# Optimization experiments

Hardware: AMD Instinct MI355X
Metric: run time of the kernel (lower is better)

## Reference

```python
import jax, jax.numpy as jnp
import numpy as np

DIM = 768
NUM_HEADS = 12
HEAD_DIM = DIM // NUM_HEADS
HW = 32  # input_size = (32, 32)


def setup_inputs() -> dict:
    key = jax.random.key(0)
    ks = jax.random.split(key, 7)
    return {
        "x": jax.random.normal(ks[0], (8, HW, HW, DIM), dtype=jnp.float32),
        "w_qkv": jax.random.normal(ks[1], (DIM, 3 * DIM), dtype=jnp.float32) * 0.02,
        "b_qkv": jnp.zeros((3 * DIM,), dtype=jnp.float32),
        "w_proj": jax.random.normal(ks[2], (DIM, DIM), dtype=jnp.float32) * 0.02,
        "b_proj": jnp.zeros((DIM,), dtype=jnp.float32),
        "rel_pos_h": jax.random.normal(ks[3], (2 * HW - 1, HEAD_DIM), dtype=jnp.float32) * 0.02,
        "rel_pos_w": jax.random.normal(ks[4], (2 * HW - 1, HEAD_DIM), dtype=jnp.float32) * 0.02,
    }


def _gather_rel_pos(size, rel_pos):
    # q_size == k_size == size, so no resize; index = i - j + (size - 1)
    idx = jnp.arange(size)[:, None] - jnp.arange(size)[None, :] + (size - 1)
    return rel_pos[idx]  # [size, size, head_dim]


def reference(x, w_qkv, b_qkv, w_proj, b_proj, rel_pos_h, rel_pos_w):
    B, H, W, C = x.shape
    nH, D = NUM_HEADS, HEAD_DIM
    scale = D ** -0.5
    S = H * W

    qkv = x.reshape(B, S, C) @ w_qkv + b_qkv          # [B,S,3C]
    qkv = qkv.reshape(B, S, 3, nH, D).transpose(2, 0, 3, 1, 4)  # [3,B,nH,S,D]
    q, k, v = qkv[0], qkv[1], qkv[2]

    attn = jnp.einsum('bnsd,bntd->bnst', q * scale, k)  # [B,nH,S,S]

    # decomposed relative positional bias
    Rh = _gather_rel_pos(H, rel_pos_h)                  # [H,H,D]
    Rw = _gather_rel_pos(W, rel_pos_w)                  # [W,W,D]
    r_q = q.reshape(B, nH, H, W, D)
    rel_h = jnp.einsum('bnhwc,hkc->bnhwk', r_q, Rh)     # [B,nH,H,W,H]
    rel_w = jnp.einsum('bnhwc,wkc->bnhwk', r_q, Rw)     # [B,nH,H,W,W]
    attn = (attn.reshape(B, nH, H, W, H, W)
            + rel_h[..., :, None]
            + rel_w[..., None, :]).reshape(B, nH, S, S)

    attn = jax.nn.softmax(attn, axis=-1)
    out = jnp.einsum('bnst,bntd->bnsd', attn, v)        # [B,nH,S,D]
    out = out.transpose(0, 2, 1, 3).reshape(B, H, W, C)
    return out @ w_proj + b_proj
```

## Files before the change

### kernel.cpp

```cpp
#include <hip/hip_runtime.h>
#include <cstdint>
#include <cstddef>

#define NH 12
#define HDIM 64
#define C_ 768
#define C3 2304
#define SEQ 1024
#define LS 72
#define LSV 76
#define SMAX 6.0f
#define LOG2E 1.4426950408889634f

typedef short bf16x8_t __attribute__((ext_vector_type(8)));
typedef float f32x4_t __attribute__((ext_vector_type(4)));
typedef unsigned short u16x4_t __attribute__((ext_vector_type(4)));

__device__ __forceinline__ unsigned short bf16_rne(float x) {
    unsigned int u = __float_as_uint(x);
    u += 0x7FFFu + ((u >> 16) & 1u);
    return (unsigned short)(u >> 16);
}
__device__ __forceinline__ float bf16f(unsigned short h) {
    return __uint_as_float(((unsigned int)h) << 16);
}

__device__ __forceinline__ void load_lds16(const unsigned short* g, unsigned short* l) {
    auto gp = (const __attribute__((address_space(1))) unsigned short*)(uintptr_t)g;
    auto lp = (__attribute__((address_space(3))) unsigned short*)(uint32_t)(uintptr_t)l;
    __builtin_amdgcn_global_load_lds(gp, lp, 16, 0, 0);
}

__device__ __forceinline__ int swz(int row, int g) {
    const int pr = row >> 1;
    const int ch = (((row & 1) << 2) | g) ^ (pr & 7);
    return pr * 64 + ch * 8;
}

__global__ __launch_bounds__(256)
void split_kernel(const float* __restrict__ in, unsigned short* __restrict__ hi)
{
    const int i = blockIdx.x * 256 + threadIdx.x;
    float4 v = ((const float4*)in)[i];
    u16x4_t h;
    h.x = bf16_rne(v.x); h.y = bf16_rne(v.y); h.z = bf16_rne(v.z); h.w = bf16_rne(v.w);
    ((u16x4_t*)hi)[i] = h;
}

__global__ __launch_bounds__(256)
void splitT_kernel(const float* __restrict__ W, unsigned short* __restrict__ Thi,
                   unsigned short* __restrict__ Tlo, int Kdim, int Ndim)
{
    __shared__ float tile[32][33];
    const int t = threadIdx.x;
    const int kb = blockIdx.y * 32, nb = blockIdx.x * 32;
    const int lr = t >> 3, lc = (t & 7) * 4;
    *(float4*)&tile[lr][lc] = *(const float4*)&W[(size_t)(kb + lr) * Ndim + nb + lc];
    __syncthreads();
    const float v0 = tile[lc + 0][lr];
    const float v1 = tile[lc + 1][lr];
    const float v2 = tile[lc + 2][lr];
    const float v3 = tile[lc + 3][lr];
    u16x4_t h, l;
    h.x = bf16_rne(v0); l.x = bf16_rne(v0 - bf16f(h.x));
    h.y = bf16_rne(v1); l.y = bf16_rne(v1 - bf16f(h.y));
    h.z = bf16_rne(v2); l.z = bf16_rne(v2 - bf16f(h.z));
    h.w = bf16_rne(v3); l.w = bf16_rne(v3 - bf16f(h.w));
    *(u16x4_t*)&Thi[(size_t)(nb + lr) * Kdim + kb + lc] = h;
    *(u16x4_t*)&Tlo[(size_t)(nb + lr) * Kdim + kb + lc] = l;
}

__global__ __launch_bounds__(256, 2)
void qkvgemm_kernel(const unsigned short* __restrict__ Ahi, const unsigned short* __restrict__ BThi,
                    const float* __restrict__ bias,
                    unsigned short* __restrict__ q_hi, unsigned short* __restrict__ k_hi,
                    unsigned short* __restrict__ v_hi)
{
    constexpr int K = 768;
    __shared__ unsigned short As[4096];
    __shared__ unsigned short Bs[4096];
    const int tid = threadIdx.x;
    const int w = tid >> 6, lane = tid & 63, g = lane >> 4, r = lane & 15;
    const int wr = (w >> 1) * 64, wc = (w & 1) * 64;

    const int bid  = blockIdx.x;
    const int xcd  = bid & 7;
    const int idx  = bid >> 3;
    const int msub = idx & 7;
    const int ntile = idx >> 3;
    const int m0 = (xcd * 8 + msub) * 128;
    const int n0 = ntile * 128;

    int row_[2], gc_[2];
#pragma unroll
    for (int i = 0; i < 2; ++i) {
        const int s = i * 256 + tid;
        const int pr = s >> 3;
        const int u = (s & 7) ^ (pr & 7);
        row_[i] = pr * 2 + (u >> 2);
        gc_[i]  = u & 3;
    }
    const unsigned short* gA0 = Ahi + (size_t)(m0 + row_[0]) * K + gc_[0] * 8;
    const unsigned short* gA1 = Ahi + (size_t)(m0 + row_[1]) * K + gc_[1] * 8;
    const unsigned short* gB0 = BThi + (size_t)(n0 + row_[0]) * K + gc_[0] * 8;
    const unsigned short* gB1 = BThi + (size_t)(n0 + row_[1]) * K + gc_[1] * 8;
    unsigned short* lA0 = As + w * 512;
    unsigned short* lA1 = As + 2048 + w * 512;
    unsigned short* lB0 = Bs + w * 512;
    unsigned short* lB1 = Bs + 2048 + w * 512;

    f32x4_t acc[4][4];
#pragma unroll
    for (int i = 0; i < 4; ++i)
#pragma unroll
        for (int j = 0; j < 4; ++j)
#pragma unroll
            for (int q = 0; q < 4; ++q) acc[i][j][q] = 0.f;

    for (int k0 = 0; k0 < K; k0 += 32) {
        __syncthreads();
        load_lds16(gA0 + k0, lA0);
        load_lds16(gA1 + k0, lA1);
        load_lds16(gB0 + k0, lB0);
        load_lds16(gB1 + k0, lB1);
        __syncthreads();
        bf16x8_t am[4];
#pragma unroll
        for (int i = 0; i < 4; ++i)
            am[i] = *(const bf16x8_t*)&As[swz(wr + 16 * i + r, g)];
#pragma unroll
        for (int j = 0; j < 4; ++j) {
            const bf16x8_t bn = *(const bf16x8_t*)&Bs[swz(wc + 16 * j + r, g)];
#pragma unroll
            for (int i = 0; i < 4; ++i)
                acc[i][j] = __builtin_amdgcn_mfma_f32_16x16x32_bf16(am[i], bn, acc[i][j], 0, 0, 0);
        }
    }

    const int third = n0 >= 1536 ? 2 : (n0 >= 768 ? 1 : 0);
    unsigned short* outH = third == 2 ? v_hi : third == 1 ? k_hi : q_hi;
#pragma unroll
    for (int j = 0; j < 4; ++j) {
        const int n = n0 + wc + 16 * j + r;
        const float bj = bias[n];
        const int nn = n - third * 768;
        const int h = nn >> 6, d = nn & 63;
#pragma unroll
        for (int i = 0; i < 4; ++i) {
            const int m = m0 + wr + 16 * i + 4 * g;
            const int b = m >> 10, t = m & 1023;
            const size_t hb = ((size_t)(b * NH + h)) << 16;
            unsigned short* dh = outH + hb + (size_t)t * 64 + d;
#pragma unroll
            for (int q = 0; q < 4; ++q)
                dh[(size_t)q * 64] = bf16_rne(acc[i][j][q] + bj);
        }
    }
}

template<int N>
__global__ __launch_bounds__(256, 2)
void gemm_mfma_kernel(const unsigned short* __restrict__ Ahi, const unsigned short* __restrict__ Alo,
                      const unsigned short* __restrict__ BThi, const unsigned short* __restrict__ BTlo,
                      const float* __restrict__ bias, float* __restrict__ C)
{
    constexpr int K = 768;
    __shared__ unsigned short As[128 * LS];
    __shared__ unsigned short Bs[128 * LS];
    const int tid = threadIdx.x;
    const int w = tid >> 6, lane = tid & 63, g = lane >> 4, r = lane & 15;
    const int wr = (w >> 1) * 64, wc = (w & 1) * 64;

    const int bid  = blockIdx.x;
    const int xcd  = bid & 7;
    const int idx  = bid >> 3;
    const int msub = idx & 7;
    const int ntile = idx >> 3;
    const int m0 = (xcd * 8 + msub) * 128;
    const int n0 = ntile * 128;

    const int srow = tid >> 1, sh = (tid & 1) * 16;

    const unsigned short* aH = Ahi + (size_t)(m0 + srow) * K + sh;
    const unsigned short* aL = Alo + (size_t)(m0 + srow) * K + sh;
    const unsigned short* bH = BThi + (size_t)(n0 + srow) * K + sh;
    const unsigned short* bL = BTlo + (size_t)(n0 + srow) * K + sh;

    f32x4_t acc[4][4];
#pragma unroll
    for (int i = 0; i < 4; ++i)
#pragma unroll
        for (int j = 0; j < 4; ++j)
#pragma unroll
            for (int q = 0; q < 4; ++q) acc[i][j][q] = 0.f;

    for (int k0 = 0; k0 < K; k0 += 32) {
        bf16x8_t va0 = *(const bf16x8_t*)(aH + k0);
        bf16x8_t va1 = *(const bf16x8_t*)(aH + k0 + 8);
        bf16x8_t wa0 = *(const bf16x8_t*)(aL + k0);
        bf16x8_t wa1 = *(const bf16x8_t*)(aL + k0 + 8);
        bf16x8_t vb0 = *(const bf16x8_t*)(bH + k0);
        bf16x8_t vb1 = *(const bf16x8_t*)(bH + k0 + 8);
        bf16x8_t wb0 = *(const bf16x8_t*)(bL + k0);
        bf16x8_t wb1 = *(const bf16x8_t*)(bL + k0 + 8);
        __syncthreads();
        *(bf16x8_t*)&As[srow * LS + sh]          = va0;
        *(bf16x8_t*)&As[srow * LS + sh + 8]      = va1;
        *(bf16x8_t*)&As[srow * LS + 32 + sh]     = wa0;
        *(bf16x8_t*)&As[srow * LS + 32 + sh + 8] = wa1;
        *(bf16x8_t*)&Bs[srow * LS + sh]          = vb0;
        *(bf16x8_t*)&Bs[srow * LS + sh + 8]      = vb1;
        *(bf16x8_t*)&Bs[srow * LS + 32 + sh]     = wb0;
        *(bf16x8_t*)&Bs[srow * LS + 32 + sh + 8] = wb1;
        __syncthreads();
        bf16x8_t amh[4], aml[4];
#pragma unroll
        for (int i = 0; i < 4; ++i) {
            amh[i] = *(const bf16x8_t*)&As[(wr + 16 * i + r) * LS + 8 * g];
            aml[i] = *(const bf16x8_t*)&As[(wr + 16 * i + r) * LS + 32 + 8 * g];
        }
#pragma unroll
        for (int j = 0; j < 4; ++j) {
            bf16x8_t bnh = *(const bf16x8_t*)&Bs[(wc + 16 * j + r) * LS + 8 * g];
            bf16x8_t bnl = *(const bf16x8_t*)&Bs[(wc + 16 * j + r) * LS + 32 + 8 * g];
#pragma unroll
            for (int i = 0; i < 4; ++i) {
                acc[i][j] = __builtin_amdgcn_mfma_f32_16x16x32_bf16(amh[i], bnh, acc[i][j], 0, 0, 0);
                acc[i][j] = __builtin_amdgcn_mfma_f32_16x16x32_bf16(amh[i], bnl, acc[i][j], 0, 0, 0);
                acc[i][j] = __builtin_amdgcn_mfma_f32_16x16x32_bf16(aml[i], bnh, acc[i][j], 0, 0, 0);
            }
        }
    }

#pragma unroll
    for (int j = 0; j < 4; ++j) {
        const float bj = bias[n0 + wc + 16 * j + r];
#pragma unroll
        for (int i = 0; i < 4; ++i) {
            float* Cp = C + (size_t)(m0 + wr + 16 * i + 4 * g) * N + n0 + wc + 16 * j + r;
#pragma unroll
            for (int q = 0; q < 4; ++q)
                Cp[(size_t)q * N] = acc[i][j][q] + bj;
        }
    }
}

__global__ __launch_bounds__(256)
void relcat_kernel(const float* __restrict__ rel_h, const float* __restrict__ rel_w,
                   unsigned short* __restrict__ relcat)
{
    const int i = blockIdx.x * 256 + threadIdx.x;
    if (i >= 2016) return;
    const int j = i * 4;
    const int row = j >> 6, col = j & 63;
    const float* src = row < 63 ? &rel_h[row * 64 + col] : &rel_w[(row - 63) * 64 + col];
    const float4 v = *(const float4*)src;
    u16x4_t h;
    h.x = bf16_rne(v.x); h.y = bf16_rne(v.y); h.z = bf16_rne(v.z); h.w = bf16_rne(v.w);
    *(u16x4_t*)&relcat[j] = h;
}

__global__ __launch_bounds__(256, 4)
void relgemm_kernel(const unsigned short* __restrict__ qhi, const unsigned short* __restrict__ relcat,
                    unsigned short* __restrict__ G)
{
    __shared__ unsigned short bs[128 * LS];
    const int tid = threadIdx.x;
    const int sb = blockIdx.x, bh = blockIdx.y;
    const int w = tid >> 6, lane = tid & 63, g = lane >> 4, r = lane & 15;
    const size_t hb = (size_t)bh << 16;

    {
        const int row = tid >> 1, c32 = (tid & 1) * 32;
        if (row < 126) {
#pragma unroll
            for (int e = 0; e < 4; ++e)
                *(bf16x8_t*)&bs[row * LS + c32 + 8 * e] =
                    *(const bf16x8_t*)&relcat[row * 64 + c32 + 8 * e];
        } else {
            const bf16x8_t z = {0,0,0,0,0,0,0,0};
#pragma unroll
            for (int e = 0; e < 4; ++e)
                *(bf16x8_t*)&bs[row * LS + c32 + 8 * e] = z;
        }
    }
    bf16x8_t aq[2][2];
#pragma unroll
    for (int i = 0; i < 2; ++i)
#pragma unroll
        for (int c = 0; c < 2; ++c)
            aq[i][c] = *(const bf16x8_t*)(qhi + hb + (size_t)(sb * 128 + w * 32 + 16 * i + r) * 64 + c * 32 + 8 * g);
    __syncthreads();

    f32x4_t acc[2][8];
#pragma unroll
    for (int i = 0; i < 2; ++i)
#pragma unroll
        for (int fj = 0; fj < 8; ++fj)
#pragma unroll
            for (int q = 0; q < 4; ++q) acc[i][fj][q] = 0.f;

#pragma unroll
    for (int c = 0; c < 2; ++c)
#pragma unroll
        for (int fj = 0; fj < 8; ++fj) {
            const bf16x8_t brel = *(const bf16x8_t*)&bs[(16 * fj + r) * LS + c * 32 + 8 * g];
#pragma unroll
            for (int i = 0; i < 2; ++i)
                acc[i][fj] = __builtin_amdgcn_mfma_f32_16x16x32_bf16(aq[i][c], brel, acc[i][fj], 0, 0, 0);
        }

    unsigned short* Gb = G + (((size_t)bh << 10) + sb * 128 + w * 32) * 128;
#pragma unroll
    for (int i = 0; i < 2; ++i)
#pragma unroll
        for (int reg = 0; reg < 4; ++reg) {
            unsigned short* Gr = Gb + (size_t)(16 * i + 4 * g + reg) * 128 + r;
#pragma unroll
            for (int fj = 0; fj < 8; ++fj)
                Gr[16 * fj] = bf16_rne(acc[i][fj][reg]);
        }
}

__global__ __launch_bounds__(256, 3)
void attn9_kernel(const unsigned short* __restrict__ qhi,
                  const unsigned short* __restrict__ khi,
                  const unsigned short* __restrict__ vhi,
                  const unsigned short* __restrict__ G,
                  unsigned short* __restrict__ outh, unsigned short* __restrict__ outl)
{
    __shared__ unsigned short ksh[2 * 64 * LS];
    __shared__ unsigned short vsh[2 * 64 * LSV];
    __shared__ unsigned short psh[64 * 64];

    const int tid  = threadIdx.x;
    const int bh   = blockIdx.x;
    const int s0   = blockIdx.y * 64;
    const int w    = tid >> 6;
    const int lane = tid & 63;
    const int g    = lane >> 4;
    const int r    = lane & 15;
    const size_t hb = (size_t)bh << 16;

    bf16x8_t aq[2];
#pragma unroll
    for (int c = 0; c < 2; ++c)
        aq[c] = *(const bf16x8_t*)(qhi + hb + (size_t)(s0 + w * 16 + r) * 64 + c * 32 + 8 * g);

    const unsigned short* Grow[4];
    int qcb[4];
    float bw[4][2];
#pragma unroll
    for (int reg = 0; reg < 4; ++reg) {
        const int row = s0 + w * 16 + 4 * g + reg;
        Grow[reg] = G + (((size_t)bh << 10) + row) * 128;
        qcb[reg] = (row >> 5) + 31;
        const int iw = row & 31;
#pragma unroll
        for (int jh = 0; jh < 2; ++jh)
            bw[reg][jh] = bf16f(Grow[reg][94 + iw - 16 * jh - r]) * LOG2E;
    }

    f32x4_t oacc[4];
    float lsum[4];
#pragma unroll
    for (int i = 0; i < 4; ++i) {
        lsum[i] = 0.f;
#pragma unroll
        for (int j = 0; j < 4; ++j) oacc[i][j] = 0.f;
    }

    const int krow = tid >> 2, kc16 = (tid & 3) * 16;
    const int tb = (tid >> 4) * 4, d0 = (tid & 15) * 4;

    {
        const unsigned short* kh = khi + hb + (size_t)krow * 64 + kc16;
        const bf16x8_t a0 = *(const bf16x8_t*)kh;
        const bf16x8_t a1 = *(const bf16x8_t*)(kh + 8);
        u16x4_t rv[4];
#pragma unroll
        for (int i = 0; i < 4; ++i)
            rv[i] = *(const u16x4_t*)(vhi + hb + (size_t)(tb + i) * 64 + d0);
        *(bf16x8_t*)&ksh[krow * LS + kc16]     = a0;
        *(bf16x8_t*)&ksh[krow * LS + kc16 + 8] = a1;
#pragma unroll
        for (int c2 = 0; c2 < 4; ++c2) {
            u16x4_t th;
            th.x = rv[0][c2]; th.y = rv[1][c2]; th.z = rv[2][c2]; th.w = rv[3][c2];
            *(u16x4_t*)&vsh[(d0 + c2) * LSV + tb] = th;
        }
    }
    __syncthreads();

    int cur = 0;
    for (int t0 = 0; t0 < SEQ; t0 += 64) {
        const int cok = cur * 64 * LS;
        const int cov = cur * 64 * LSV;
        const int tn = (t0 + 64 < SEQ) ? t0 + 64 : t0;
        bf16x8_t nk0, nk1;
        u16x4_t nv[4];
        {
            const unsigned short* kh = khi + hb + (size_t)(tn + krow) * 64 + kc16;
            nk0 = *(const bf16x8_t*)kh;
            nk1 = *(const bf16x8_t*)(kh + 8);
#pragma unroll
            for (int i = 0; i < 4; ++i)
                nv[i] = *(const u16x4_t*)(vhi + hb + (size_t)(tn + tb + i) * 64 + d0);
        }

        f32x4_t sacc[4];
#pragma unroll
        for (int fj = 0; fj < 4; ++fj)
#pragma unroll
            for (int j = 0; j < 4; ++j) sacc[fj][j] = 0.f;
#pragma unroll
        for (int c = 0; c < 2; ++c)
#pragma unroll
            for (int fj = 0; fj < 4; ++fj) {
                const bf16x8_t bkh = *(const bf16x8_t*)&ksh[cok + (16 * fj + r) * LS + c * 32 + 8 * g];
                sacc[fj] = __builtin_amdgcn_mfma_f32_16x16x32_bf16(aq[c], bkh, sacc[fj], 0, 0, 0);
            }

        const int kh0 = t0 >> 5;
        float bh0[4], bh1[4];
#pragma unroll
        for (int reg = 0; reg < 4; ++reg) {
            bh0[reg] = (bf16f(Grow[reg][qcb[reg] - kh0])     - SMAX) * LOG2E;
            bh1[reg] = (bf16f(Grow[reg][qcb[reg] - kh0 - 1]) - SMAX) * LOG2E;
        }
#pragma unroll
        for (int fj = 0; fj < 4; ++fj)
#pragma unroll
            for (int reg = 0; reg < 4; ++reg) {
                const float s = fmaf(sacc[fj][reg], 0.125f * LOG2E,
                                     ((fj >> 1) ? bh1[reg] : bh0[reg]) + bw[reg][fj & 1]);
                const float e = exp2f(s);
                sacc[fj][reg] = e;
                lsum[reg] += e;
            }

#pragma unroll
        for (int fj = 0; fj < 4; ++fj)
#pragma unroll
            for (int reg = 0; reg < 4; ++reg) {
                const int row = w * 16 + 4 * g + reg;
                const int addr = row * 64 + (((2 * fj + (r >> 3)) ^ (row & 7)) << 3) + (r & 7);
                psh[addr] = bf16_rne(sacc[fj][reg]);
            }
        asm volatile("s_waitcnt lgkmcnt(0)" ::: "memory");
        __builtin_amdgcn_sched_barrier(0);

#pragma unroll
        for (int c = 0; c < 2; ++c) {
            const int prow = w * 16 + r;
            const int paddr = prow * 64 + (((4 * c + g) ^ (prow & 7)) << 3);
            const bf16x8_t aph = *(const bf16x8_t*)&psh[paddr];
#pragma unroll
            for (int fd = 0; fd < 4; ++fd) {
                const bf16x8_t bvh = *(const bf16x8_t*)&vsh[cov + (16 * fd + r) * LSV + c * 32 + 8 * g];
                oacc[fd] = __builtin_amdgcn_mfma_f32_16x16x32_bf16(aph, bvh, oacc[fd], 0, 0, 0);
            }
        }

        const int nok = (cur ^ 1) * 64 * LS;
        const int nov = (cur ^ 1) * 64 * LSV;
        *(bf16x8_t*)&ksh[nok + krow * LS + kc16]     = nk0;
        *(bf16x8_t*)&ksh[nok + krow * LS + kc16 + 8] = nk1;
#pragma unroll
        for (int c2 = 0; c2 < 4; ++c2) {
            u16x4_t th;
            th.x = nv[0][c2]; th.y = nv[1][c2]; th.z = nv[2][c2]; th.w = nv[3][c2];
            *(u16x4_t*)&vsh[nov + (d0 + c2) * LSV + tb] = th;
        }
        __syncthreads();
        cur ^= 1;
    }

    const int b = bh / NH, h = bh - (bh / NH) * NH;
#pragma unroll
    for (int reg = 0; reg < 4; ++reg) {
        float rs = lsum[reg];
#pragma unroll
        for (int off = 1; off < 16; off <<= 1) rs += __shfl_xor(rs, off);
        const float rinv = 1.f / rs;
        const int qrow = s0 + w * 16 + 4 * g + reg;
        unsigned short* oph = outh + ((size_t)b * SEQ + qrow) * C_ + h * HDIM;
        unsigned short* opl = outl + ((size_t)b * SEQ + qrow) * C_ + h * HDIM;
#pragma unroll
        for (int fd = 0; fd < 4; ++fd) {
            const float v = oacc[fd][reg] * rinv;
            const unsigned short hv = bf16_rne(v);
            oph[16 * fd + r] = hv;
            opl[16 * fd + r] = bf16_rne(v - bf16f(hv));
        }
    }
}

extern "C" void kernel_launch(void* const* d_in, const int* in_sizes, int n_in,
                              void* d_out, int out_size, void* d_ws, size_t ws_size,
                              hipStream_t stream) {
    (void)in_sizes; (void)n_in; (void)out_size; (void)ws_size;
    const float* x      = (const float*)d_in[0];
    const float* w_qkv  = (const float*)d_in[1];
    const float* b_qkv  = (const float*)d_in[2];
    const float* w_proj = (const float*)d_in[3];
    const float* b_proj = (const float*)d_in[4];
    const float* rel_h  = (const float*)d_in[5];
    const float* rel_w  = (const float*)d_in[6];
    float* out = (float*)d_out;

    char* base = (char*)d_ws;
    unsigned short* xhi    = (unsigned short*)(base + 0);
    unsigned short* xlo    = (unsigned short*)(base + 12582912);
    unsigned short* wqh    = (unsigned short*)(base + 25165824);
    unsigned short* wql    = (unsigned short*)(base + 28704768);
    unsigned short* wph    = (unsigned short*)(base + 32243712);
    unsigned short* wpl    = (unsigned short*)(base + 33423360);
    unsigned short* qhi    = (unsigned short*)(base + 34603008);
    unsigned short* relcat = (unsigned short*)(base + 47185920);
    unsigned short* khi    = (unsigned short*)(base + 59768832);
    unsigned short* vhi    = (unsigned short*)(base + 84934656);
    unsigned short* G      = (unsigned short*)(base + 110100480);
    unsigned short* ohif   = xhi;
    unsigned short* olo    = xlo;

    split_kernel<<<6144, 256, 0, stream>>>(x, xhi);
    {
        dim3 gq(C3 / 32, C_ / 32);
        splitT_kernel<<<gq, 256, 0, stream>>>(w_qkv, wqh, wql, C_, C3);
        dim3 gp(C_ / 32, C_ / 32);
        splitT_kernel<<<gp, 256, 0, stream>>>(w_proj, wph, wpl, C_, C_);
        relcat_kernel<<<8, 256, 0, stream>>>(rel_h, rel_w, relcat);
    }
    qkvgemm_kernel<<<1152, 256, 0, stream>>>(xhi, wqh, b_qkv, qhi, khi, vhi);
    {
        dim3 grid(8, 96);
        relgemm_kernel<<<grid, 256, 0, stream>>>(qhi, relcat, G);
    }
    {
        dim3 grid(96, SEQ / 64);
        attn9_kernel<<<grid, 256, 0, stream>>>(qhi, khi, vhi, G, ohif, olo);
    }
    gemm_mfma_kernel<C_><<<384, 256, 0, stream>>>(ohif, olo, wph, wpl, b_proj, out);
}
```

Baseline: 182.8 us.

## Transpose attention MFMA operands and pass P through registers via ds_bpermute

The attention kernel swaps the A/B operands of the QK^T and PV MFMAs so each lane holds one query row's scores. The probability tile is then packed with v_cvt_pk_bf16_f32 and rearranged across lanes with ds_bpermute, which removes the P shared-memory buffer and its write/wait/read round-trip. This also simplifies the bias loads to one row per lane, reduces the softmax row-sum shuffles and vectorises the output stores. The smaller LDS footprint allows a launch bound of four blocks per CU instead of three, at the cost of extra bpermute and select instructions and higher register pressure.

```diff
diff --git a/kernel.cpp b/kernel.cpp
--- a/kernel.cpp
+++ b/kernel.cpp
@@ -322,16 +322,15 @@
         }
 }
 
-__global__ __launch_bounds__(256, 3)
-void attn9_kernel(const unsigned short* __restrict__ qhi,
-                  const unsigned short* __restrict__ khi,
-                  const unsigned short* __restrict__ vhi,
-                  const unsigned short* __restrict__ G,
-                  unsigned short* __restrict__ outh, unsigned short* __restrict__ outl)
+__global__ __launch_bounds__(256, 4)
+void attn10_kernel(const unsigned short* __restrict__ qhi,
+                   const unsigned short* __restrict__ khi,
+                   const unsigned short* __restrict__ vhi,
+                   const unsigned short* __restrict__ G,
+                   unsigned short* __restrict__ outh, unsigned short* __restrict__ outl)
 {
     __shared__ unsigned short ksh[2 * 64 * LS];
     __shared__ unsigned short vsh[2 * 64 * LSV];
-    __shared__ unsigned short psh[64 * 64];
 
     const int tid  = threadIdx.x;
     const int bh   = blockIdx.x;
@@ -347,19 +346,17 @@
     for (int c = 0; c < 2; ++c)
         aq[c] = *(const bf16x8_t*)(qhi + hb + (size_t)(s0 + w * 16 + r) * 64 + c * 32 + 8 * g);
 
-    const unsigned short* Grow[4];
-    int qcb[4];
+    const unsigned short* Gbh = G + ((size_t)bh << 17);
+    const int q    = s0 + w * 16 + r;
+    const int qoff = q * 128;
+    const int qcb  = (q >> 5) + 31;
+    const int iw   = q & 31;
     float bw[4][2];
 #pragma unroll
-    for (int reg = 0; reg < 4; ++reg) {
-        const int row = s0 + w * 16 + 4 * g + reg;
-        Grow[reg] = G + (((size_t)bh << 10) + row) * 128;
-        qcb[reg] = (row >> 5) + 31;
-        const int iw = row & 31;
+    for (int reg = 0; reg < 4; ++reg)
 #pragma unroll
         for (int jh = 0; jh < 2; ++jh)
-            bw[reg][jh] = bf16f(Grow[reg][94 + iw - 16 * jh - r]) * LOG2E;
-    }
+            bw[reg][jh] = bf16f(Gbh[qoff + 94 + iw - 16 * jh - 4 * g - reg]) * LOG2E;
 
     f32x4_t oacc[4];
     float lsum[4];
@@ -372,6 +369,9 @@
 
     const int krow = tid >> 2, kc16 = (tid & 3) * 16;
     const int tb = (tid >> 4) * 4, d0 = (tid & 15) * 4;
+    const int addr_a = (((g & 1) << 5) + r) << 2;
+    const int addr_b = addr_a + 64;
+    const bool lowg = g < 2;
 
     {
         const unsigned short* kh = khi + hb + (size_t)krow * 64 + kc16;
@@ -418,47 +418,49 @@
 #pragma unroll
             for (int fj = 0; fj < 4; ++fj) {
                 const bf16x8_t bkh = *(const bf16x8_t*)&ksh[cok + (16 * fj + r) * LS + c * 32 + 8 * g];
-                sacc[fj] = __builtin_amdgcn_mfma_f32_16x16x32_bf16(aq[c], bkh, sacc[fj], 0, 0, 0);
+                sacc[fj] = __builtin_amdgcn_mfma_f32_16x16x32_bf16(bkh, aq[c], sacc[fj], 0, 0, 0);
             }
 
         const int kh0 = t0 >> 5;
-        float bh0[4], bh1[4];
-#pragma unroll
-        for (int reg = 0; reg < 4; ++reg) {
-            bh0[reg] = (bf16f(Grow[reg][qcb[reg] - kh0])     - SMAX) * LOG2E;
-            bh1[reg] = (bf16f(Grow[reg][qcb[reg] - kh0 - 1]) - SMAX) * LOG2E;
-        }
+        const float bh0 = (bf16f(Gbh[qoff + qcb - kh0])     - SMAX) * LOG2E;
+        const float bh1 = (bf16f(Gbh[qoff + qcb - kh0 - 1]) - SMAX) * LOG2E;
 #pragma unroll
         for (int fj = 0; fj < 4; ++fj)
 #pragma unroll
             for (int reg = 0; reg < 4; ++reg) {
                 const float s = fmaf(sacc[fj][reg], 0.125f * LOG2E,
-                                     ((fj >> 1) ? bh1[reg] : bh0[reg]) + bw[reg][fj & 1]);
+                                     ((fj >> 1) ? bh1 : bh0) + bw[reg][fj & 1]);
                 const float e = exp2f(s);
                 sacc[fj][reg] = e;
                 lsum[reg] += e;
             }
 
-#pragma unroll
-        for (int fj = 0; fj < 4; ++fj)
-#pragma unroll
-            for (int reg = 0; reg < 4; ++reg) {
-                const int row = w * 16 + 4 * g + reg;
-                const int addr = row * 64 + (((2 * fj + (r >> 3)) ^ (row & 7)) << 3) + (r & 7);
-                psh[addr] = bf16_rne(sacc[fj][reg]);
-            }
-        asm volatile("s_waitcnt lgkmcnt(0)" ::: "memory");
-        __builtin_amdgcn_sched_barrier(0);
+        unsigned int pk01[4], pk23[4];
+#pragma unroll
+        for (int fj = 0; fj < 4; ++fj) {
+            asm("v_cvt_pk_bf16_f32 %0, %1, %2" : "=v"(pk01[fj]) : "v"(sacc[fj][0]), "v"(sacc[fj][1]));
+            asm("v_cvt_pk_bf16_f32 %0, %1, %2" : "=v"(pk23[fj]) : "v"(sacc[fj][2]), "v"(sacc[fj][3]));
+        }
 
 #pragma unroll
         for (int c = 0; c < 2; ++c) {
-            const int prow = w * 16 + r;
-            const int paddr = prow * 64 + (((4 * c + g) ^ (prow & 7)) << 3);
-            const bf16x8_t aph = *(const bf16x8_t*)&psh[paddr];
+            const int a01A = __builtin_amdgcn_ds_bpermute(addr_a, (int)pk01[2 * c]);
+            const int a23A = __builtin_amdgcn_ds_bpermute(addr_a, (int)pk23[2 * c]);
+            const int b01A = __builtin_amdgcn_ds_bpermute(addr_b, (int)pk01[2 * c]);
+            const int b23A = __builtin_amdgcn_ds_bpermute(addr_b, (int)pk23[2 * c]);
+            const int a01B = __builtin_amdgcn_ds_bpermute(addr_a, (int)pk01[2 * c + 1]);
+            const int a23B = __builtin_amdgcn_ds_bpermute(addr_a, (int)pk23[2 * c + 1]);
+            const int b01B = __builtin_amdgcn_ds_bpermute(addr_b, (int)pk01[2 * c + 1]);
+            const int b23B = __builtin_amdgcn_ds_bpermute(addr_b, (int)pk23[2 * c + 1]);
+            union { int u[4]; bf16x8_t v; } pf;
+            pf.u[0] = lowg ? a01A : a01B;
+            pf.u[1] = lowg ? a23A : a23B;
+            pf.u[2] = lowg ? b01A : b01B;
+            pf.u[3] = lowg ? b23A : b23B;
 #pragma unroll
             for (int fd = 0; fd < 4; ++fd) {
                 const bf16x8_t bvh = *(const bf16x8_t*)&vsh[cov + (16 * fd + r) * LSV + c * 32 + 8 * g];
-                oacc[fd] = __builtin_amdgcn_mfma_f32_16x16x32_bf16(aph, bvh, oacc[fd], 0, 0, 0);
+                oacc[fd] = __builtin_amdgcn_mfma_f32_16x16x32_bf16(bvh, pf.v, oacc[fd], 0, 0, 0);
             }
         }
 
@@ -477,22 +479,24 @@
     }
 
     const int b = bh / NH, h = bh - (bh / NH) * NH;
-#pragma unroll
-    for (int reg = 0; reg < 4; ++reg) {
-        float rs = lsum[reg];
-#pragma unroll
-        for (int off = 1; off < 16; off <<= 1) rs += __shfl_xor(rs, off);
-        const float rinv = 1.f / rs;
-        const int qrow = s0 + w * 16 + 4 * g + reg;
-        unsigned short* oph = outh + ((size_t)b * SEQ + qrow) * C_ + h * HDIM;
-        unsigned short* opl = outl + ((size_t)b * SEQ + qrow) * C_ + h * HDIM;
-#pragma unroll
-        for (int fd = 0; fd < 4; ++fd) {
+    float rs = (lsum[0] + lsum[1]) + (lsum[2] + lsum[3]);
+    rs += __shfl_xor(rs, 16);
+    rs += __shfl_xor(rs, 32);
+    const float rinv = 1.f / rs;
+    unsigned short* oph = outh + ((size_t)b * SEQ + q) * C_ + h * HDIM + 4 * g;
+    unsigned short* opl = outl + ((size_t)b * SEQ + q) * C_ + h * HDIM + 4 * g;
+#pragma unroll
+    for (int fd = 0; fd < 4; ++fd) {
+        u16x4_t hv, lv;
+#pragma unroll
+        for (int reg = 0; reg < 4; ++reg) {
             const float v = oacc[fd][reg] * rinv;
-            const unsigned short hv = bf16_rne(v);
-            oph[16 * fd + r] = hv;
-            opl[16 * fd + r] = bf16_rne(v - bf16f(hv));
-        }
+            const unsigned short hh = bf16_rne(v);
+            hv[reg] = hh;
+            lv[reg] = bf16_rne(v - bf16f(hh));
+        }
+        *(u16x4_t*)(oph + 16 * fd) = hv;
+        *(u16x4_t*)(opl + 16 * fd) = lv;
     }
 }
 
@@ -539,7 +543,7 @@
     }
     {
         dim3 grid(96, SEQ / 64);
-        attn9_kernel<<<grid, 256, 0, stream>>>(qhi, khi, vhi, G, ohif, olo);
+        attn10_kernel<<<grid, 256, 0, stream>>>(qhi, khi, vhi, G, ohif, olo);
     }
     gemm_mfma_kernel<C_><<<384, 256, 0, stream>>>(ohif, olo, wph, wpl, b_proj, out);
 }
```

Result: faster. 178.8 us (-2.2%).
